# Kernel tuning notes

Measured on AMD Instinct MI355X. Metric: run time of the kernel, lower is better.

## Reference

```python
import jax, jax.numpy as jnp
import numpy as np

K = 1024
D = 256
COMMITMENT_WEIGHT = 0.25


def setup_inputs() -> dict:
    key = jax.random.key(0)
    kz, kw = jax.random.split(key)
    z = jax.random.normal(kz, (16, 4096, D), dtype=jnp.float32)
    # nn.init.uniform_(weight, -1/K, 1/K)
    emb = jax.random.uniform(kw, (K, D), dtype=jnp.float32, minval=-1.0 / K, maxval=1.0 / K)
    return {"z": z, "emb": emb}


def reference(z, emb):
    B, N, _ = z.shape
    flat = z.reshape(-1, D)                                  # [BN, D]
    dist = (jnp.sum(flat * flat, axis=1, keepdims=True)
            - 2.0 * flat @ emb.T
            + jnp.sum(emb * emb, axis=1))                    # [BN, K]
    indices = jnp.argmin(dist, axis=1)                       # [BN]
    z_q = emb[indices].reshape(z.shape)                      # [B, N, D]
    codebook_loss = jnp.mean((z_q - jax.lax.stop_gradient(z)) ** 2)
    commitment_loss = jnp.mean((z - jax.lax.stop_gradient(z_q)) ** 2)
    loss = codebook_loss + COMMITMENT_WEIGHT * commitment_loss
    z_q_st = z + jax.lax.stop_gradient(z_q - z)              # straight-through
    return z_q_st, loss, indices.reshape(B, N)
```

## Files before the change

### kernel.cpp

```cpp
#include <hip/hip_runtime.h>


constexpr int D      = 256;
constexpr int KC     = 1024;
constexpr int BM     = 64;
constexpr int BN     = 64;
constexpr int NROWS  = 16 * 4096;
constexpr long long ZQ_N = (long long)NROWS * D;
constexpr float MARGIN = 2e-4f;
constexpr int  CAP   = 32768;

__device__ __forceinline__ float np_half_sumsq(const float* a, int s) {
    float r[8];
#pragma unroll
    for (int j = 0; j < 8; ++j) r[j] = __fmul_rn(a[j * s], a[j * s]);
    for (int i = 8; i < 128; i += 8)
#pragma unroll
        for (int j = 0; j < 8; ++j)
            r[j] = __fadd_rn(r[j], __fmul_rn(a[(i + j) * s], a[(i + j) * s]));
    return __fadd_rn(__fadd_rn(__fadd_rn(r[0], r[1]), __fadd_rn(r[2], r[3])),
                     __fadd_rn(__fadd_rn(r[4], r[5]), __fadd_rn(r[6], r[7])));
}
__device__ __forceinline__ float np_sumsq_256(const float* a, int s) {
    return __fadd_rn(np_half_sumsq(a, s), np_half_sumsq(a + 128 * s, s));
}

__global__ __launch_bounds__(256) void vq_prep(const float* __restrict__ emb,
                                               float* __restrict__ se32,
                                               double* __restrict__ acc,
                                               int* __restrict__ cnt) {
    int k = blockIdx.x * 256 + threadIdx.x;
    if (k < KC) se32[k] = np_sumsq_256(emb + (size_t)k * D, 1);
    if (k == 0) { *acc = 0.0; *cnt = 0; }
}

__global__ __launch_bounds__(256) void vq_main(const float* __restrict__ z,
                                               const float* __restrict__ emb,
                                               const float* __restrict__ se32,
                                               float* __restrict__ out_zq,
                                               float* __restrict__ out_idx1,
                                               float* __restrict__ out_idx2,
                                               double* __restrict__ acc,
                                               int* __restrict__ cnt,
                                               int* __restrict__ rowlist) {
    __shared__ float xs[D][BM];
    __shared__ float es[32][BN];
    __shared__ float red_sec[BM * 16];
    __shared__ float sxs[BM];
    __shared__ int   code_of_row[BM];
    __shared__ float wave_part[4];

    const int tid = threadIdx.x;
    const int tx  = tid & 15;
    const int ty  = tid >> 4;
    const int r0  = blockIdx.x * BM;

    {
        int r = tid >> 2;
        int dbase = (tid & 3) << 6;
        const float* zp = z + (size_t)(r0 + r) * D + dbase;
#pragma unroll
        for (int j = 0; j < 16; ++j) {
            float4 v = *(const float4*)(zp + 4 * j);
            int d = dbase + 4 * j;
            xs[d + 0][r] = v.x; xs[d + 1][r] = v.y;
            xs[d + 2][r] = v.z; xs[d + 3][r] = v.w;
        }
    }
    __syncthreads();
    if (tid < BM) sxs[tid] = np_sumsq_256(&xs[0][tid], BM);

    float bestv[4], secv[4];
    int   bestk[4];
#pragma unroll
    for (int i = 0; i < 4; ++i) { bestv[i] = 3.0e38f; secv[i] = 3.0e38f; bestk[i] = 0; }

    for (int kt = 0; kt < KC / BN; ++kt) {
        const int k0 = kt * BN;
        float a[4][4];
#pragma unroll
        for (int i = 0; i < 4; ++i)
#pragma unroll
            for (int j = 0; j < 4; ++j) a[i][j] = 0.f;

        for (int dc = 0; dc < D / 32; ++dc) {
            const int d0 = dc * 32;
            __syncthreads();
            {
                int c  = tid >> 2;
                int dd = (tid & 3) << 3;
                const float* ep = emb + (size_t)(k0 + c) * D + d0 + dd;
                float4 v0 = *(const float4*)(ep);
                float4 v1 = *(const float4*)(ep + 4);
                es[dd + 0][c] = v0.x; es[dd + 1][c] = v0.y;
                es[dd + 2][c] = v0.z; es[dd + 3][c] = v0.w;
                es[dd + 4][c] = v1.x; es[dd + 5][c] = v1.y;
                es[dd + 6][c] = v1.z; es[dd + 7][c] = v1.w;
            }
            __syncthreads();
#pragma unroll
            for (int kk = 0; kk < 32; ++kk) {
                float4 xv = *(const float4*)&xs[d0 + kk][ty << 2];
                float4 ev = *(const float4*)&es[kk][tx << 2];
                float xr[4] = { xv.x, xv.y, xv.z, xv.w };
                float er[4] = { ev.x, ev.y, ev.z, ev.w };
#pragma unroll
                for (int i = 0; i < 4; ++i)
#pragma unroll
                    for (int j = 0; j < 4; ++j)
                        a[i][j] = fmaf(xr[i], er[j], a[i][j]);
            }
        }
#pragma unroll
        for (int j = 0; j < 4; ++j) {
            int k = k0 + (tx << 2) + j;
            float se = se32[k];
#pragma unroll
            for (int i = 0; i < 4; ++i) {
                float t = (sxs[(ty << 2) + i] - 2.0f * a[i][j]) + se;
                if (t < bestv[i]) { secv[i] = bestv[i]; bestv[i] = t; bestk[i] = k; }
                else if (t < secv[i]) { secv[i] = t; }
            }
        }
    }

    __syncthreads();
    float* red_val = &es[0][0];
    int*   red_idx = (int*)&es[16][0];
#pragma unroll
    for (int i = 0; i < 4; ++i) {
        int r = (ty << 2) + i;
        red_val[r * 16 + tx] = bestv[i];
        red_idx[r * 16 + tx] = bestk[i];
        red_sec[r * 16 + tx] = secv[i];
    }
    __syncthreads();
    if (tid < BM) {
        int r = tid;
        float b1 = 3.0e38f; int k1 = 1 << 30; int t1 = 0;
#pragma unroll
        for (int t = 0; t < 16; ++t) {
            float v  = red_val[r * 16 + t];
            int   id = red_idx[r * 16 + t];
            if (v < b1 || (v == b1 && id < k1)) { b1 = v; k1 = id; t1 = t; }
        }
        float b2 = 3.0e38f;
#pragma unroll
        for (int t = 0; t < 16; ++t) {
            float v = (t == t1) ? red_sec[r * 16 + t] : red_val[r * 16 + t];
            if (v < b2) b2 = v;
        }
        code_of_row[r] = k1;
        out_idx1[r0 + r] = (float)k1;
        out_idx2[r0 + r] = (float)k1;
        if (b2 - b1 <= MARGIN) {
            int slot = atomicAdd(cnt, 1);
            if (slot < CAP) rowlist[slot] = r0 + r;
        }
    }
    __syncthreads();

    float ls = 0.f;
    {
        int r = tid >> 2;
        int dbase = (tid & 3) << 6;
        int c = code_of_row[r];
        const float* ep = emb + (size_t)c * D + dbase;
        float* op = out_zq + (size_t)(r0 + r) * D + dbase;
#pragma unroll
        for (int j = 0; j < 16; ++j) {
            float4 e4 = *(const float4*)(ep + 4 * j);
            int d = dbase + 4 * j;
            float d0v = e4.x - xs[d + 0][r];
            float d1v = e4.y - xs[d + 1][r];
            float d2v = e4.z - xs[d + 2][r];
            float d3v = e4.w - xs[d + 3][r];
            ls += d0v * d0v + d1v * d1v + d2v * d2v + d3v * d3v;
            *(float4*)(op + 4 * j) = e4;
        }
    }
#pragma unroll
    for (int off = 32; off > 0; off >>= 1) ls += __shfl_down(ls, off);
    if ((tid & 63) == 0) wave_part[tid >> 6] = ls;
    __syncthreads();
    if (tid == 0) {
        double t = (double)wave_part[0] + (double)wave_part[1]
                 + (double)wave_part[2] + (double)wave_part[3];
        atomicAdd(acc, t);
    }
}

__global__ __launch_bounds__(256) void vq_rescore(const float* __restrict__ z,
                                                  const float* __restrict__ emb,
                                                  const float* __restrict__ se32,
                                                  float* __restrict__ out_idx1,
                                                  float* __restrict__ out_idx2,
                                                  const int* __restrict__ rowlist,
                                                  const int* __restrict__ cnt) {
    int gw   = (blockIdx.x * blockDim.x + threadIdx.x) >> 6;
    int nw   = (gridDim.x * blockDim.x) >> 6;
    int lane = threadIdx.x & 63;
    int n = *cnt; if (n > CAP) n = CAP;
    for (int li = gw; li < n; li += nw) {
        int row = rowlist[li];
        const float*  x  = z + (size_t)row * D;
        const float4* xp = (const float4*)x;
        float sx = np_sumsq_256(x, 1);
        float bt = 3.0e38f; int bk = 1 << 30;
        for (int c = 0; c < 16; ++c) {
            int k = c * 64 + lane;
            const float4* ep = (const float4*)(emb + (size_t)k * D);
            double s = 0.0;
#pragma unroll 8
            for (int q = 0; q < 64; ++q) {
                float4 ev = ep[q];
                float4 xv = xp[q];
                s = fma((double)xv.x, (double)ev.x, s);
                s = fma((double)xv.y, (double)ev.y, s);
                s = fma((double)xv.z, (double)ev.z, s);
                s = fma((double)xv.w, (double)ev.w, s);
            }
            float g = (float)s;
            float t = __fadd_rn(__fsub_rn(sx, 2.0f * g), se32[k]);
            if (t < bt) { bt = t; bk = k; }
        }
#pragma unroll
        for (int off = 32; off > 0; off >>= 1) {
            float ot = __shfl_xor(bt, off);
            int   ok = __shfl_xor(bk, off);
            if (ot < bt || (ot == bt && ok < bk)) { bt = ot; bk = ok; }
        }
        if (lane == 0) { out_idx1[row] = (float)bk; out_idx2[row] = (float)bk; }
    }
}

__global__ void vq_finalize(const double* __restrict__ acc,
                            float* __restrict__ l1, float* __restrict__ l2) {
    double m = *acc / (double)ZQ_N;
    float v = (float)(1.25 * m);
    *l1 = v; *l2 = v;
}

extern "C" void kernel_launch(void* const* d_in, const int* in_sizes, int n_in,
                              void* d_out, int out_size, void* d_ws, size_t ws_size,
                              hipStream_t stream) {
    const float* z   = (const float*)d_in[0];
    const float* emb = (const float*)d_in[1];
    float* out = (float*)d_out;

    float* out_zq    = out;
    float* out_loss1 = out + ZQ_N;
    float* out_idx1  = out + ZQ_N + 1;
    size_t osz = (size_t)out_size;
    float* out_idx2  = out + (osz - (size_t)NROWS);
    float* out_loss2 = out + (osz - (size_t)NROWS - 1);

    float*  se32    = (float*)d_ws;
    double* acc     = (double*)((char*)d_ws + 4096);
    int*    cnt     = (int*)((char*)d_ws + 4104);
    int*    rowlist = (int*)((char*)d_ws + 8192);

    vq_prep<<<4, 256, 0, stream>>>(emb, se32, acc, cnt);
    vq_main<<<NROWS / BM, 256, 0, stream>>>(z, emb, se32, out_zq, out_idx1,
                                            out_idx2, acc, cnt, rowlist);
    vq_rescore<<<256, 256, 0, stream>>>(z, emb, se32, out_idx1, out_idx2,
                                        rowlist, cnt);
    vq_finalize<<<1, 1, 0, stream>>>(acc, out_loss1, out_loss2);
}
```

Measured before the change: 1.510 ms.

## Enlarge distance GEMM tile to 128x128 with double-buffered register-prefetched chunks

The distance matmul tile grows from 64x64 with 4x4 per-thread outputs to 128x128 with 8x8 per-thread outputs. Both z and emb are streamed in 16-deep chunks through double-buffered padded shared memory, with the next chunk prefetched into registers while the current one is computed. This raises arithmetic intensity and reduces syncs and global reloads. The loss is now taken from the best distance value instead of recomputing squared differences, and the rescore margin is halved, which affects accuracy near ties and how many rows get rescored. Register pressure rises and launch bounds request 3 blocks per CU.

Result: slower. 2.088 ms (+38.2%).

```diff
diff --git a/kernel.cpp b/kernel.cpp
--- a/kernel.cpp
+++ b/kernel.cpp
@@ -3,11 +3,13 @@
 
 constexpr int D      = 256;
 constexpr int KC     = 1024;
-constexpr int BM     = 64;
-constexpr int BN     = 64;
+constexpr int BM     = 128;
+constexpr int BN     = 128;
+constexpr int DC     = 16;
+constexpr int PAD    = 132;
 constexpr int NROWS  = 16 * 4096;
 constexpr long long ZQ_N = (long long)NROWS * D;
-constexpr float MARGIN = 2e-4f;
+constexpr float MARGIN = 1e-4f;
 constexpr int  CAP   = 32768;
 
 __device__ __forceinline__ float np_half_sumsq(const float* a, int s) {
@@ -34,107 +36,133 @@
     if (k == 0) { *acc = 0.0; *cnt = 0; }
 }
 
-__global__ __launch_bounds__(256) void vq_main(const float* __restrict__ z,
-                                               const float* __restrict__ emb,
-                                               const float* __restrict__ se32,
-                                               float* __restrict__ out_zq,
-                                               float* __restrict__ out_idx1,
-                                               float* __restrict__ out_idx2,
-                                               double* __restrict__ acc,
-                                               int* __restrict__ cnt,
-                                               int* __restrict__ rowlist) {
-    __shared__ float xs[D][BM];
-    __shared__ float es[32][BN];
-    __shared__ float red_sec[BM * 16];
+__global__ __launch_bounds__(256, 3) void vq_main(const float* __restrict__ z,
+                                                  const float* __restrict__ emb,
+                                                  const float* __restrict__ se32,
+                                                  float* __restrict__ out_zq,
+                                                  float* __restrict__ out_idx1,
+                                                  float* __restrict__ out_idx2,
+                                                  double* __restrict__ acc,
+                                                  int* __restrict__ cnt,
+                                                  int* __restrict__ rowlist) {
+    __shared__ float xs_c[2][DC][PAD];
+    __shared__ float es_c[2][DC][PAD];
     __shared__ float sxs[BM];
     __shared__ int   code_of_row[BM];
-    __shared__ float wave_part[4];
 
     const int tid = threadIdx.x;
     const int tx  = tid & 15;
     const int ty  = tid >> 4;
     const int r0  = blockIdx.x * BM;
 
+    if (tid < BM) sxs[tid] = np_sumsq_256(z + (size_t)(r0 + tid) * D, 1);
+
+    const int scol = tid >> 1;
+    const int soff = (tid & 1) * 8;
+
     {
-        int r = tid >> 2;
-        int dbase = (tid & 3) << 6;
-        const float* zp = z + (size_t)(r0 + r) * D + dbase;
-#pragma unroll
-        for (int j = 0; j < 16; ++j) {
-            float4 v = *(const float4*)(zp + 4 * j);
-            int d = dbase + 4 * j;
-            xs[d + 0][r] = v.x; xs[d + 1][r] = v.y;
-            xs[d + 2][r] = v.z; xs[d + 3][r] = v.w;
-        }
-    }
-    __syncthreads();
-    if (tid < BM) sxs[tid] = np_sumsq_256(&xs[0][tid], BM);
-
-    float bestv[4], secv[4];
-    int   bestk[4];
-#pragma unroll
-    for (int i = 0; i < 4; ++i) { bestv[i] = 3.0e38f; secv[i] = 3.0e38f; bestk[i] = 0; }
-
-    for (int kt = 0; kt < KC / BN; ++kt) {
-        const int k0 = kt * BN;
-        float a[4][4];
-#pragma unroll
-        for (int i = 0; i < 4; ++i)
-#pragma unroll
-            for (int j = 0; j < 4; ++j) a[i][j] = 0.f;
-
-        for (int dc = 0; dc < D / 32; ++dc) {
-            const int d0 = dc * 32;
+        const float* zp = z + (size_t)(r0 + scol) * D + soff;
+        float4 a0 = *(const float4*)zp, a1 = *(const float4*)(zp + 4);
+        const float* ep = emb + (size_t)scol * D + soff;
+        float4 b0 = *(const float4*)ep, b1 = *(const float4*)(ep + 4);
+        const float* af = (const float*)&a0; const float* af1 = (const float*)&a1;
+        const float* bf = (const float*)&b0; const float* bf1 = (const float*)&b1;
+#pragma unroll
+        for (int e = 0; e < 4; ++e) {
+            xs_c[0][soff + e][scol]     = af[e];
+            xs_c[0][soff + 4 + e][scol] = af1[e];
+            es_c[0][soff + e][scol]     = bf[e];
+            es_c[0][soff + 4 + e][scol] = bf1[e];
+        }
+    }
+    __syncthreads();
+
+    float sxr[8];
+#pragma unroll
+    for (int i = 0; i < 8; ++i)
+        sxr[i] = sxs[(i < 4) ? (ty * 4 + i) : (64 + ty * 4 + i - 4)];
+
+    float bestv[8], secv[8];
+    int   bestk[8];
+#pragma unroll
+    for (int i = 0; i < 8; ++i) { bestv[i] = 3.0e38f; secv[i] = 3.0e38f; bestk[i] = 0; }
+
+    float a[8][8];
+#pragma unroll
+    for (int i = 0; i < 8; ++i)
+#pragma unroll
+        for (int j = 0; j < 8; ++j) a[i][j] = 0.f;
+
+    int cur = 0;
+    for (int ci = 0; ci < 128; ++ci) {
+        float4 nx0, nx1, ne0, ne1;
+        const bool have = (ci + 1 < 128);
+        if (have) {
+            int nkt = (ci + 1) >> 4, nd0 = ((ci + 1) & 15) * DC;
+            const float* zp = z + (size_t)(r0 + scol) * D + nd0 + soff;
+            nx0 = *(const float4*)zp; nx1 = *(const float4*)(zp + 4);
+            const float* ep = emb + (size_t)(nkt * BN + scol) * D + nd0 + soff;
+            ne0 = *(const float4*)ep; ne1 = *(const float4*)(ep + 4);
+        }
+#pragma unroll
+        for (int kk = 0; kk < DC; ++kk) {
+            float4 xlo = *(const float4*)&xs_c[cur][kk][ty << 2];
+            float4 xhi = *(const float4*)&xs_c[cur][kk][64 + (ty << 2)];
+            float4 elo = *(const float4*)&es_c[cur][kk][tx << 2];
+            float4 ehi = *(const float4*)&es_c[cur][kk][64 + (tx << 2)];
+            float xr[8] = { xlo.x, xlo.y, xlo.z, xlo.w, xhi.x, xhi.y, xhi.z, xhi.w };
+            float er[8] = { elo.x, elo.y, elo.z, elo.w, ehi.x, ehi.y, ehi.z, ehi.w };
+#pragma unroll
+            for (int i = 0; i < 8; ++i)
+#pragma unroll
+                for (int j = 0; j < 8; ++j)
+                    a[i][j] = fmaf(xr[i], er[j], a[i][j]);
+        }
+        if ((ci & 15) == 15) {
+            int kt = ci >> 4;
+#pragma unroll
+            for (int j = 0; j < 8; ++j) {
+                int c = (j < 4) ? (tx * 4 + j) : (64 + tx * 4 + j - 4);
+                float se = se32[kt * BN + c];
+#pragma unroll
+                for (int i = 0; i < 8; ++i) {
+                    float t = __fadd_rn(__fsub_rn(sxr[i], 2.0f * a[i][j]), se);
+                    if (t < bestv[i]) { secv[i] = bestv[i]; bestv[i] = t; bestk[i] = kt * BN + c; }
+                    else if (t < secv[i]) { secv[i] = t; }
+                    a[i][j] = 0.f;
+                }
+            }
+        }
+        __syncthreads();
+        if (have) {
+            int nb = cur ^ 1;
+            const float* af = (const float*)&nx0; const float* af1 = (const float*)&nx1;
+            const float* bf = (const float*)&ne0; const float* bf1 = (const float*)&ne1;
+#pragma unroll
+            for (int e = 0; e < 4; ++e) {
+                xs_c[nb][soff + e][scol]     = af[e];
+                xs_c[nb][soff + 4 + e][scol] = af1[e];
+                es_c[nb][soff + e][scol]     = bf[e];
+                es_c[nb][soff + 4 + e][scol] = bf1[e];
+            }
+            cur = nb;
             __syncthreads();
-            {
-                int c  = tid >> 2;
-                int dd = (tid & 3) << 3;
-                const float* ep = emb + (size_t)(k0 + c) * D + d0 + dd;
-                float4 v0 = *(const float4*)(ep);
-                float4 v1 = *(const float4*)(ep + 4);
-                es[dd + 0][c] = v0.x; es[dd + 1][c] = v0.y;
-                es[dd + 2][c] = v0.z; es[dd + 3][c] = v0.w;
-                es[dd + 4][c] = v1.x; es[dd + 5][c] = v1.y;
-                es[dd + 6][c] = v1.z; es[dd + 7][c] = v1.w;
-            }
-            __syncthreads();
-#pragma unroll
-            for (int kk = 0; kk < 32; ++kk) {
-                float4 xv = *(const float4*)&xs[d0 + kk][ty << 2];
-                float4 ev = *(const float4*)&es[kk][tx << 2];
-                float xr[4] = { xv.x, xv.y, xv.z, xv.w };
-                float er[4] = { ev.x, ev.y, ev.z, ev.w };
-#pragma unroll
-                for (int i = 0; i < 4; ++i)
-#pragma unroll
-                    for (int j = 0; j < 4; ++j)
-                        a[i][j] = fmaf(xr[i], er[j], a[i][j]);
-            }
-        }
-#pragma unroll
-        for (int j = 0; j < 4; ++j) {
-            int k = k0 + (tx << 2) + j;
-            float se = se32[k];
-#pragma unroll
-            for (int i = 0; i < 4; ++i) {
-                float t = (sxs[(ty << 2) + i] - 2.0f * a[i][j]) + se;
-                if (t < bestv[i]) { secv[i] = bestv[i]; bestv[i] = t; bestk[i] = k; }
-                else if (t < secv[i]) { secv[i] = t; }
-            }
-        }
-    }
-
-    __syncthreads();
-    float* red_val = &es[0][0];
-    int*   red_idx = (int*)&es[16][0];
-#pragma unroll
-    for (int i = 0; i < 4; ++i) {
-        int r = (ty << 2) + i;
+        }
+    }
+
+    __syncthreads();
+    float* red_val = (float*)&xs_c[0][0][0];
+    float* red_sec = red_val + 2048;
+    int*   red_idx = (int*)&es_c[0][0][0];
+#pragma unroll
+    for (int i = 0; i < 8; ++i) {
+        int r = (i < 4) ? (ty * 4 + i) : (64 + ty * 4 + i - 4);
         red_val[r * 16 + tx] = bestv[i];
+        red_sec[r * 16 + tx] = secv[i];
         red_idx[r * 16 + tx] = bestk[i];
-        red_sec[r * 16 + tx] = secv[i];
-    }
-    __syncthreads();
+    }
+    __syncthreads();
+    float row_b1 = 0.f;
     if (tid < BM) {
         int r = tid;
         float b1 = 3.0e38f; int k1 = 1 << 30; int t1 = 0;
@@ -153,40 +181,25 @@
         code_of_row[r] = k1;
         out_idx1[r0 + r] = (float)k1;
         out_idx2[r0 + r] = (float)k1;
+        row_b1 = b1;
         if (b2 - b1 <= MARGIN) {
             int slot = atomicAdd(cnt, 1);
             if (slot < CAP) rowlist[slot] = r0 + r;
         }
     }
-    __syncthreads();
-
-    float ls = 0.f;
+#pragma unroll
+    for (int off = 32; off > 0; off >>= 1) row_b1 += __shfl_down(row_b1, off);
+    if (tid < BM && (tid & 63) == 0) atomicAdd(acc, (double)row_b1);
+    __syncthreads();
+
     {
-        int r = tid >> 2;
-        int dbase = (tid & 3) << 6;
-        int c = code_of_row[r];
-        const float* ep = emb + (size_t)c * D + dbase;
-        float* op = out_zq + (size_t)(r0 + r) * D + dbase;
-#pragma unroll
-        for (int j = 0; j < 16; ++j) {
-            float4 e4 = *(const float4*)(ep + 4 * j);
-            int d = dbase + 4 * j;
-            float d0v = e4.x - xs[d + 0][r];
-            float d1v = e4.y - xs[d + 1][r];
-            float d2v = e4.z - xs[d + 2][r];
-            float d3v = e4.w - xs[d + 3][r];
-            ls += d0v * d0v + d1v * d1v + d2v * d2v + d3v * d3v;
-            *(float4*)(op + 4 * j) = e4;
-        }
-    }
-#pragma unroll
-    for (int off = 32; off > 0; off >>= 1) ls += __shfl_down(ls, off);
-    if ((tid & 63) == 0) wave_part[tid >> 6] = ls;
-    __syncthreads();
-    if (tid == 0) {
-        double t = (double)wave_part[0] + (double)wave_part[1]
-                 + (double)wave_part[2] + (double)wave_part[3];
-        atomicAdd(acc, t);
+        int r = tid >> 1;
+        int h = (tid & 1) * 128;
+        const float* ep = emb + (size_t)code_of_row[r] * D + h;
+        float* op = out_zq + (size_t)(r0 + r) * D + h;
+#pragma unroll
+        for (int q = 0; q < 32; ++q)
+            *(float4*)(op + 4 * q) = *(const float4*)(ep + 4 * q);
     }
 }
 
@@ -263,7 +276,7 @@
     vq_prep<<<4, 256, 0, stream>>>(emb, se32, acc, cnt);
     vq_main<<<NROWS / BM, 256, 0, stream>>>(z, emb, se32, out_zq, out_idx1,
                                             out_idx2, acc, cnt, rowlist);
-    vq_rescore<<<256, 256, 0, stream>>>(z, emb, se32, out_idx1, out_idx2,
+    vq_rescore<<<512, 256, 0, stream>>>(z, emb, se32, out_idx1, out_idx2,
                                         rowlist, cnt);
     vq_finalize<<<1, 1, 0, stream>>>(acc, out_loss1, out_loss2);
 }
```
